# Kernel optimization log

Measured on AMD Instinct MI355X. Metric: run time of the kernel, lower is better.

Reference implementation:

```python
import jax, jax.numpy as jnp
import numpy as np

LUT_SIZE = 4096
TWO_PI = 2.0 * np.pi


def _lut_tables():
    idx = jnp.arange(LUT_SIZE, dtype=jnp.float32)
    ang = idx * (TWO_PI / LUT_SIZE)
    return jnp.sin(ang), jnp.cos(ang)


def lut_sin_cos(theta):
    """4096-entry LUT sin/cos with linear interpolation, period 2*pi."""
    sin_t, cos_t = _lut_tables()
    fidx = theta * (LUT_SIZE / TWO_PI)
    i0f = jnp.floor(fidx)
    w = fidx - i0f  # interpolation weight in [0,1)
    i0 = jnp.mod(i0f.astype(jnp.int32), LUT_SIZE)
    i1 = jnp.mod(i0 + 1, LUT_SIZE)
    s = sin_t[i0] * (1.0 - w) + sin_t[i1] * w
    c = cos_t[i0] * (1.0 - w) + cos_t[i1] * w
    return s, c


def setup_inputs() -> dict:
    key = jax.random.key(0)
    ks = jax.random.split(key, 9)
    B_, D, N = 32, 1024, 2048
    return {
        "x_real": jax.random.normal(ks[0], (B_, D), jnp.float32),
        "x_imag": jax.random.normal(ks[1], (B_, D), jnp.float32),
        "t": jax.random.uniform(ks[2], (B_,), jnp.float32),
        "input_proj_w": jax.random.normal(ks[3], (D, 2 * D), jnp.float32) * (1.0 / np.sqrt(2 * D)),
        "input_proj_b": jnp.zeros((D,), jnp.float32),
        "W": jax.random.normal(ks[4], (N, D), jnp.float32) * 0.02,
        "B": jnp.zeros((N, D), jnp.float32),
        "out_real_w": jax.random.normal(ks[5], (D, N), jnp.float32) * (1.0 / np.sqrt(N)),
        "out_imag_w": jax.random.normal(ks[6], (D, N), jnp.float32) * (1.0 / np.sqrt(N)),
    }


def reference(x_real, x_imag, t, input_proj_w, input_proj_b, W, B, out_real_w, out_imag_w):
    # input projection on concatenated real/imag: (batch, d_model)
    x_combined = jnp.concatenate([x_real, x_imag], axis=-1)
    x_collapsed = x_combined @ input_proj_w.T + input_proj_b
    # broadcast: (batch, 1, d) / (n, d) + (n, d) + (batch, 1, 1)
    wavelength = 1.0 + jnp.abs(W)
    theta = x_collapsed[:, None, :] / wavelength + B + t[:, None, None]
    sin_theta, cos_theta = lut_sin_cos(theta)
    cos_sum = cos_theta.sum(axis=-1)  # (batch, n)
    sin_sum = sin_theta.sum(axis=-1)
    out_real = cos_sum @ out_real_w.T
    out_imag = sin_sum @ out_imag_w.T
    return jax.nn.silu(out_real), jax.nn.silu(out_imag)
```

## Files before the change

kernel.cpp:

```cpp
#include <hip/hip_runtime.h>
#include <math.h>

#define D_MODEL 1024
#define N_RES   2048
#define BATCH   32
constexpr float INV_2PI = 0.15915494309189535f;

#define WS_XC 0
#define WS_CS (32 * 1024)
#define WS_SS (WS_CS + 32 * 2048)
#define WS_PA (WS_SS + 32 * 2048)
#define WS_PR (WS_PA + 2 * 32 * 1024)
#define WS_PI (WS_PR + 4 * 32 * 1024)

__global__ __launch_bounds__(256) void kA_partial(const float* __restrict__ xr,
                                                  const float* __restrict__ xi,
                                                  const float* __restrict__ ipw,
                                                  float* __restrict__ pa) {
  const int tid  = threadIdx.x;
  const int lane = tid & 63;
  const int wave = tid >> 6;
  const int d0 = (blockIdx.x & 255) * 4;
  const int kc = blockIdx.x >> 8;
  const int b0 = wave * 8;

  const float4* x4p  = (const float4*)(kc ? xi : xr);
  const float4* ipw4 = (const float4*)ipw;
  const int woff = kc * 256;

  float acc[8][4];
#pragma unroll
  for (int b = 0; b < 8; ++b)
#pragma unroll
    for (int d = 0; d < 4; ++d) acc[b][d] = 0.f;

#pragma unroll 1
  for (int i = 0; i < 4; ++i) {
    const int j = lane + 64 * i;
    float4 w4[4];
#pragma unroll
    for (int d = 0; d < 4; ++d) w4[d] = ipw4[(d0 + d) * 512 + woff + j];
#pragma unroll
    for (int b = 0; b < 8; ++b) {
      float4 x4 = x4p[(b0 + b) * 256 + j];
#pragma unroll
      for (int d = 0; d < 4; ++d) {
        acc[b][d] += x4.x * w4[d].x + x4.y * w4[d].y + x4.z * w4[d].z + x4.w * w4[d].w;
      }
    }
  }

#pragma unroll
  for (int b = 0; b < 8; ++b) {
#pragma unroll
    for (int d = 0; d < 4; ++d) {
      float v = acc[b][d];
#pragma unroll
      for (int m = 32; m >= 1; m >>= 1) v += __shfl_xor(v, m, 64);
      if (lane == 0) pa[(size_t)(kc * BATCH + b0 + b) * D_MODEL + d0 + d] = v;
    }
  }
}

__global__ __launch_bounds__(256) void kA2(const float* __restrict__ pa,
                                           const float* __restrict__ bias,
                                           float* __restrict__ xc) {
  const int idx = blockIdx.x * 256 + threadIdx.x;
  const float4* pa4 = (const float4*)pa;
  const float4* b4p = (const float4*)bias;
  float4 a = pa4[idx];
  float4 b = pa4[8192 + idx];
  float4 c = b4p[idx & 255];
  float4 r;
  r.x = a.x + b.x + c.x;
  r.y = a.y + b.y + c.y;
  r.z = a.z + b.z + c.z;
  r.w = a.w + b.w + c.w;
  ((float4*)xc)[idx] = r;
}

__global__ __launch_bounds__(256) void kB(const float* __restrict__ xc,
                                          const float* __restrict__ W,
                                          const float* __restrict__ Bm,
                                          const float* __restrict__ t,
                                          float* __restrict__ cos_sum,
                                          float* __restrict__ sin_sum) {
  __shared__ float a_s[D_MODEL];
  __shared__ float c_s[D_MODEL];
  const int n   = blockIdx.x;
  const int tid = threadIdx.x;

  {
    const float4* W4 = (const float4*)(W + (size_t)n * D_MODEL);
    const float4* B4 = (const float4*)(Bm + (size_t)n * D_MODEL);
    float4 w4 = W4[tid];
    float4 b4 = B4[tid];
    float4 a4, c4;
    a4.x = INV_2PI / (1.f + fabsf(w4.x));
    a4.y = INV_2PI / (1.f + fabsf(w4.y));
    a4.z = INV_2PI / (1.f + fabsf(w4.z));
    a4.w = INV_2PI / (1.f + fabsf(w4.w));
    c4.x = b4.x * INV_2PI;
    c4.y = b4.y * INV_2PI;
    c4.z = b4.z * INV_2PI;
    c4.w = b4.w * INV_2PI;
    ((float4*)a_s)[tid] = a4;
    ((float4*)c_s)[tid] = c4;
  }
  __syncthreads();

  const int lane = tid & 63;
  const int wave = tid >> 6;
  const int b0 = wave * 8;
  const float4* as4 = (const float4*)a_s;
  const float4* cs4 = (const float4*)c_s;

#pragma unroll 1
  for (int bb = 0; bb < 8; ++bb) {
    const int b = b0 + bb;
    const float t2 = t[b] * INV_2PI;
    const float4* x4p = (const float4*)(xc + (size_t)b * D_MODEL);
    float ss = 0.f, cc = 0.f;
#pragma unroll
    for (int i = 0; i < 4; ++i) {
      const int j = lane + 64 * i;
      float4 x4 = x4p[j];
      float4 a4 = as4[j];
      float4 c4 = cs4[j];
      {
        float r = x4.x * a4.x + c4.x + t2;
        float fr = r - floorf(r);
        ss += __builtin_amdgcn_sinf(fr);
        cc += __builtin_amdgcn_cosf(fr);
      }
      {
        float r = x4.y * a4.y + c4.y + t2;
        float fr = r - floorf(r);
        ss += __builtin_amdgcn_sinf(fr);
        cc += __builtin_amdgcn_cosf(fr);
      }
      {
        float r = x4.z * a4.z + c4.z + t2;
        float fr = r - floorf(r);
        ss += __builtin_amdgcn_sinf(fr);
        cc += __builtin_amdgcn_cosf(fr);
      }
      {
        float r = x4.w * a4.w + c4.w + t2;
        float fr = r - floorf(r);
        ss += __builtin_amdgcn_sinf(fr);
        cc += __builtin_amdgcn_cosf(fr);
      }
    }
#pragma unroll
    for (int m = 32; m >= 1; m >>= 1) {
      ss += __shfl_xor(ss, m, 64);
      cc += __shfl_xor(cc, m, 64);
    }
    if (lane == 0) {
      cos_sum[(size_t)b * N_RES + n] = cc;
      sin_sum[(size_t)b * N_RES + n] = ss;
    }
  }
}

__global__ __launch_bounds__(256) void kC_partial(const float* __restrict__ cos_sum,
                                                  const float* __restrict__ sin_sum,
                                                  const float* __restrict__ orw,
                                                  const float* __restrict__ oiw,
                                                  float* __restrict__ pr,
                                                  float* __restrict__ pi) {
  const int tid  = threadIdx.x;
  const int lane = tid & 63;
  const int wave = tid >> 6;
  const int d0 = (blockIdx.x & 255) * 4;
  const int kc = blockIdx.x >> 8;
  const int b0 = wave * 8;
  const int jbase = kc * 128;

  float ar[8][4], ai[8][4];
#pragma unroll
  for (int b = 0; b < 8; ++b)
#pragma unroll
    for (int d = 0; d < 4; ++d) { ar[b][d] = 0.f; ai[b][d] = 0.f; }

#pragma unroll 1
  for (int i = 0; i < 2; ++i) {
    const int j = jbase + lane + 64 * i;
    float4 wr[4], wi[4];
#pragma unroll
    for (int d = 0; d < 4; ++d) {
      wr[d] = ((const float4*)(orw + (size_t)(d0 + d) * N_RES))[j];
      wi[d] = ((const float4*)(oiw + (size_t)(d0 + d) * N_RES))[j];
    }
#pragma unroll
    for (int b = 0; b < 8; ++b) {
      float4 cs = ((const float4*)(cos_sum + (size_t)(b0 + b) * N_RES))[j];
      float4 sn = ((const float4*)(sin_sum + (size_t)(b0 + b) * N_RES))[j];
#pragma unroll
      for (int d = 0; d < 4; ++d) {
        ar[b][d] += cs.x * wr[d].x + cs.y * wr[d].y + cs.z * wr[d].z + cs.w * wr[d].w;
        ai[b][d] += sn.x * wi[d].x + sn.y * wi[d].y + sn.z * wi[d].z + sn.w * wi[d].w;
      }
    }
  }

#pragma unroll
  for (int b = 0; b < 8; ++b) {
#pragma unroll
    for (int d = 0; d < 4; ++d) {
      float vr = ar[b][d];
      float vi = ai[b][d];
#pragma unroll
      for (int m = 32; m >= 1; m >>= 1) {
        vr += __shfl_xor(vr, m, 64);
        vi += __shfl_xor(vi, m, 64);
      }
      if (lane == 0) {
        const size_t o = (size_t)(kc * BATCH + b0 + b) * D_MODEL + d0 + d;
        pr[o] = vr;
        pi[o] = vi;
      }
    }
  }
}

__device__ __forceinline__ float silu(float v) { return v / (1.f + __expf(-v)); }

__global__ __launch_bounds__(256) void kC2(const float* __restrict__ pr,
                                           const float* __restrict__ pi,
                                           float* __restrict__ out) {
  const int idx = blockIdx.x * 256 + threadIdx.x;
  const float4* pr4 = (const float4*)pr;
  const float4* pi4 = (const float4*)pi;
  float4 vr = pr4[idx];
  float4 vi = pi4[idx];
#pragma unroll
  for (int kc = 1; kc < 4; ++kc) {
    float4 a = pr4[kc * 8192 + idx];
    float4 b = pi4[kc * 8192 + idx];
    vr.x += a.x; vr.y += a.y; vr.z += a.z; vr.w += a.w;
    vi.x += b.x; vi.y += b.y; vi.z += b.z; vi.w += b.w;
  }
  float4 orr, oii;
  orr.x = silu(vr.x); orr.y = silu(vr.y); orr.z = silu(vr.z); orr.w = silu(vr.w);
  oii.x = silu(vi.x); oii.y = silu(vi.y); oii.z = silu(vi.z); oii.w = silu(vi.w);
  ((float4*)out)[idx] = orr;
  ((float4*)out)[8192 + idx] = oii;
}

extern "C" void kernel_launch(void* const* d_in, const int* in_sizes, int n_in,
                              void* d_out, int out_size, void* d_ws, size_t ws_size,
                              hipStream_t stream) {
  const float* xr   = (const float*)d_in[0];
  const float* xi   = (const float*)d_in[1];
  const float* t    = (const float*)d_in[2];
  const float* ipw  = (const float*)d_in[3];
  const float* bias = (const float*)d_in[4];
  const float* W    = (const float*)d_in[5];
  const float* Bm   = (const float*)d_in[6];
  const float* orw  = (const float*)d_in[7];
  const float* oiw  = (const float*)d_in[8];
  float* out = (float*)d_out;

  float* ws      = (float*)d_ws;
  float* xc      = ws + WS_XC;
  float* cos_sum = ws + WS_CS;
  float* sin_sum = ws + WS_SS;
  float* pa      = ws + WS_PA;
  float* pr      = ws + WS_PR;
  float* pi      = ws + WS_PI;

  kA_partial<<<512, 256, 0, stream>>>(xr, xi, ipw, pa);
  kA2<<<32, 256, 0, stream>>>(pa, bias, xc);
  kB<<<N_RES, 256, 0, stream>>>(xc, W, Bm, t, cos_sum, sin_sum);
  kC_partial<<<1024, 256, 0, stream>>>(cos_sum, sin_sum, orw, oiw, pr, pi);
  kC2<<<32, 256, 0, stream>>>(pr, pi, out);
}
```

Before: 163.5 us.

## Keep per-row W/B factors in registers and prefetch next batch row in kB

```diff
diff --git a/kernel.cpp b/kernel.cpp
--- a/kernel.cpp
+++ b/kernel.cpp
@@ -85,82 +85,89 @@
                                           const float* __restrict__ t,
                                           float* __restrict__ cos_sum,
                                           float* __restrict__ sin_sum) {
-  __shared__ float a_s[D_MODEL];
-  __shared__ float c_s[D_MODEL];
-  const int n   = blockIdx.x;
-  const int tid = threadIdx.x;
-
-  {
-    const float4* W4 = (const float4*)(W + (size_t)n * D_MODEL);
-    const float4* B4 = (const float4*)(Bm + (size_t)n * D_MODEL);
-    float4 w4 = W4[tid];
-    float4 b4 = B4[tid];
-    float4 a4, c4;
-    a4.x = INV_2PI / (1.f + fabsf(w4.x));
-    a4.y = INV_2PI / (1.f + fabsf(w4.y));
-    a4.z = INV_2PI / (1.f + fabsf(w4.z));
-    a4.w = INV_2PI / (1.f + fabsf(w4.w));
-    c4.x = b4.x * INV_2PI;
-    c4.y = b4.y * INV_2PI;
-    c4.z = b4.z * INV_2PI;
-    c4.w = b4.w * INV_2PI;
-    ((float4*)a_s)[tid] = a4;
-    ((float4*)c_s)[tid] = c4;
-  }
-  __syncthreads();
-
+  const int n    = blockIdx.x;
+  const int tid  = threadIdx.x;
   const int lane = tid & 63;
   const int wave = tid >> 6;
-  const int b0 = wave * 8;
-  const float4* as4 = (const float4*)a_s;
-  const float4* cs4 = (const float4*)c_s;
+  const int b0   = wave * 8;
+
+  const float4* W4 = (const float4*)(W + (size_t)n * D_MODEL);
+  const float4* B4 = (const float4*)(Bm + (size_t)n * D_MODEL);
+  float4 av[4], cv[4];
+#pragma unroll
+  for (int i = 0; i < 4; ++i) {
+    float4 w4 = W4[lane + 64 * i];
+    float4 b4 = B4[lane + 64 * i];
+    av[i].x = INV_2PI / (1.f + fabsf(w4.x));
+    av[i].y = INV_2PI / (1.f + fabsf(w4.y));
+    av[i].z = INV_2PI / (1.f + fabsf(w4.z));
+    av[i].w = INV_2PI / (1.f + fabsf(w4.w));
+    cv[i].x = b4.x * INV_2PI;
+    cv[i].y = b4.y * INV_2PI;
+    cv[i].z = b4.z * INV_2PI;
+    cv[i].w = b4.w * INV_2PI;
+  }
+
+  float t2v[8];
+#pragma unroll
+  for (int bb = 0; bb < 8; ++bb) t2v[bb] = t[b0 + bb] * INV_2PI;
+
+  float4 xcur[4], xnxt[4];
+  {
+    const float4* x0 = (const float4*)(xc + (size_t)b0 * D_MODEL);
+#pragma unroll
+    for (int i = 0; i < 4; ++i) xcur[i] = x0[lane + 64 * i];
+  }
 
 #pragma unroll 1
   for (int bb = 0; bb < 8; ++bb) {
-    const int b = b0 + bb;
-    const float t2 = t[b] * INV_2PI;
-    const float4* x4p = (const float4*)(xc + (size_t)b * D_MODEL);
-    float ss = 0.f, cc = 0.f;
+    if (bb < 7) {
+      const float4* xn = (const float4*)(xc + (size_t)(b0 + bb + 1) * D_MODEL);
+#pragma unroll
+      for (int i = 0; i < 4; ++i) xnxt[i] = xn[lane + 64 * i];
+    }
+    const float t2 = t2v[bb];
+    float ss0 = 0.f, ss1 = 0.f, cc0 = 0.f, cc1 = 0.f;
 #pragma unroll
     for (int i = 0; i < 4; ++i) {
-      const int j = lane + 64 * i;
-      float4 x4 = x4p[j];
-      float4 a4 = as4[j];
-      float4 c4 = cs4[j];
-      {
-        float r = x4.x * a4.x + c4.x + t2;
-        float fr = r - floorf(r);
-        ss += __builtin_amdgcn_sinf(fr);
-        cc += __builtin_amdgcn_cosf(fr);
-      }
-      {
-        float r = x4.y * a4.y + c4.y + t2;
-        float fr = r - floorf(r);
-        ss += __builtin_amdgcn_sinf(fr);
-        cc += __builtin_amdgcn_cosf(fr);
-      }
-      {
-        float r = x4.z * a4.z + c4.z + t2;
-        float fr = r - floorf(r);
-        ss += __builtin_amdgcn_sinf(fr);
-        cc += __builtin_amdgcn_cosf(fr);
-      }
-      {
-        float r = x4.w * a4.w + c4.w + t2;
-        float fr = r - floorf(r);
-        ss += __builtin_amdgcn_sinf(fr);
-        cc += __builtin_amdgcn_cosf(fr);
-      }
-    }
+      float4 x4 = xcur[i];
+      float4 a4 = av[i];
+      float4 c4 = cv[i];
+      {
+        float r = __builtin_amdgcn_fractf(x4.x * a4.x + c4.x + t2);
+        ss0 += __builtin_amdgcn_sinf(r);
+        cc0 += __builtin_amdgcn_cosf(r);
+      }
+      {
+        float r = __builtin_amdgcn_fractf(x4.y * a4.y + c4.y + t2);
+        ss1 += __builtin_amdgcn_sinf(r);
+        cc1 += __builtin_amdgcn_cosf(r);
+      }
+      {
+        float r = __builtin_amdgcn_fractf(x4.z * a4.z + c4.z + t2);
+        ss0 += __builtin_amdgcn_sinf(r);
+        cc0 += __builtin_amdgcn_cosf(r);
+      }
+      {
+        float r = __builtin_amdgcn_fractf(x4.w * a4.w + c4.w + t2);
+        ss1 += __builtin_amdgcn_sinf(r);
+        cc1 += __builtin_amdgcn_cosf(r);
+      }
+    }
+    float ss = ss0 + ss1;
+    float cc = cc0 + cc1;
 #pragma unroll
     for (int m = 32; m >= 1; m >>= 1) {
       ss += __shfl_xor(ss, m, 64);
       cc += __shfl_xor(cc, m, 64);
     }
     if (lane == 0) {
+      const int b = b0 + bb;
       cos_sum[(size_t)b * N_RES + n] = cc;
       sin_sum[(size_t)b * N_RES + n] = ss;
     }
+#pragma unroll
+    for (int i = 0; i < 4; ++i) xcur[i] = xnxt[i];
   }
 }
 
```

After: 169.0 us. 3.3% more time.
